# Optimization experiments

Measured on AMD Instinct MI355X. Metric: run time of the kernel, lower is better.

Reference implementation:

```python
import jax, jax.numpy as jnp
import numpy as np

C = 512
NUM_GROUPS = 32
EPS = 1e-6


def setup_inputs() -> dict:
    key = jax.random.key(0)
    ks = jax.random.split(key, 10)
    x = jax.random.normal(ks[0], (2, C, 64, 64), dtype=jnp.float32)
    s = 1.0 / np.sqrt(C)
    return {
        "x": x,
        "gn_gamma": jnp.ones((C,), jnp.float32),
        "gn_beta": jnp.zeros((C,), jnp.float32),
        "wq": jax.random.normal(ks[1], (C, C), jnp.float32) * s,
        "bq": jnp.zeros((C,), jnp.float32),
        "wk": jax.random.normal(ks[2], (C, C), jnp.float32) * s,
        "bk": jnp.zeros((C,), jnp.float32),
        "wv": jax.random.normal(ks[3], (C, C), jnp.float32) * s,
        "bv": jnp.zeros((C,), jnp.float32),
        "wo": jax.random.normal(ks[4], (C, C), jnp.float32) * s,
        "bo": jnp.zeros((C,), jnp.float32),
    }


def group_norm(x, gamma, beta):
    b, c, h, w = x.shape
    xg = x.reshape(b, NUM_GROUPS, c // NUM_GROUPS, h, w)
    mean = xg.mean(axis=(2, 3, 4), keepdims=True)
    var = xg.var(axis=(2, 3, 4), keepdims=True)
    xg = (xg - mean) * jax.lax.rsqrt(var + EPS)
    x = xg.reshape(b, c, h, w)
    return x * gamma[None, :, None, None] + beta[None, :, None, None]


def conv1x1(x, w, bias):
    # 1x1 conv == channel matmul: (b,c,h,w),(o,c) -> (b,o,h,w)
    return jnp.einsum('bchw,oc->bohw', x, w) + bias[None, :, None, None]


def reference(x, gn_gamma, gn_beta, wq, bq, wk, bk, wv, bv, wo, bo):
    b, c, h, w = x.shape
    hn = group_norm(x, gn_gamma, gn_beta)
    q = conv1x1(hn, wq, bq).reshape(b, c, h * w)  # (b,c,n)
    k = conv1x1(hn, wk, bk).reshape(b, c, h * w)
    v = conv1x1(hn, wv, bv).reshape(b, c, h * w)
    scale = int(c) ** (-0.5)
    # scores[b,i,j] = sum_c q[b,c,i] k[b,c,j]
    scores = jnp.einsum('bci,bcj->bij', q, k) * scale
    attn = jax.nn.softmax(scores, axis=2)
    out = jnp.einsum('bcj,bij->bci', v, attn).reshape(b, c, h, w)
    out = conv1x1(out, wo, bo)
    return x + out
```

## Files before the change

### kernel.cpp

```cpp
#include <hip/hip_runtime.h>

typedef unsigned short ushort_t;
typedef unsigned char uchar_t;
typedef __bf16 bf16x8 __attribute__((ext_vector_type(8)));
typedef float f32x4 __attribute__((ext_vector_type(4)));

__device__ __forceinline__ ushort_t f2bf(float f) {
  unsigned u = __float_as_uint(f);
  u += 0x7fff + ((u >> 16) & 1);
  return (ushort_t)(u >> 16);
}

__device__ __forceinline__ void gload16(const void* g, void* l) {
  __builtin_amdgcn_global_load_lds(
      (const __attribute__((address_space(1))) unsigned int*)g,
      (__attribute__((address_space(3))) unsigned int*)l, 16, 0, 0);
}

__global__ __launch_bounds__(256) void cvt_weights(
    const float* __restrict__ wq, const float* __restrict__ wk,
    const float* __restrict__ wv, const float* __restrict__ wo,
    const float* __restrict__ bq, const float* __restrict__ bk,
    ushort_t* __restrict__ dst, float* __restrict__ qkbias,
    float* __restrict__ stats2) {
  int b = blockIdx.x, t = threadIdx.x;
  if (b < 1024) {
    int i = b * 256 + t;
    dst[i]          = f2bf(wq[i]);
    dst[262144 + i] = f2bf(wk[i]);
    dst[524288 + i] = f2bf(wv[i]);
    dst[786432 + i] = f2bf(wo[i]);
  } else if (b < 1028) {
    int j = (b - 1024) * 256 + t;
    qkbias[j] = (j < 512) ? bq[j] : bk[j - 512];
  } else {
    if (t < 128) stats2[t] = 0.f;
  }
}

__global__ __launch_bounds__(256) void zero_f32(float* __restrict__ p) {
  p[blockIdx.x * 256 + threadIdx.x] = 0.f;
}

__global__ __launch_bounds__(256) void gn_stats_partial(const float* __restrict__ x,
                                                        float* __restrict__ stats2) {
  int bg = blockIdx.x >> 2, q = blockIdx.x & 3;
  const float4* p = (const float4*)(x + (size_t)bg * 65536 + q * 16384);
  float s = 0.f, ss = 0.f;
  for (int i = threadIdx.x; i < 4096; i += 256) {
    float4 v = p[i];
    s += v.x + v.y + v.z + v.w;
    ss += v.x * v.x + v.y * v.y + v.z * v.z + v.w * v.w;
  }
  for (int off = 32; off; off >>= 1) {
    s += __shfl_xor(s, off, 64);
    ss += __shfl_xor(ss, off, 64);
  }
  __shared__ float sh[8];
  int wave = threadIdx.x >> 6, lane = threadIdx.x & 63;
  if (lane == 0) { sh[wave] = s; sh[4 + wave] = ss; }
  __syncthreads();
  if (threadIdx.x == 0) {
    atomicAdd(&stats2[bg * 2], sh[0] + sh[1] + sh[2] + sh[3]);
    atomicAdd(&stats2[bg * 2 + 1], sh[4] + sh[5] + sh[6] + sh[7]);
  }
}

__global__ __launch_bounds__(64) void gn_finalize(const float* __restrict__ stats2,
                                                  float* __restrict__ stats) {
  int t = threadIdx.x;
  float s = stats2[t * 2], ss = stats2[t * 2 + 1];
  float mean = s * (1.f / 65536.f);
  float var = ss * (1.f / 65536.f) - mean * mean;
  stats[t * 2] = mean;
  stats[t * 2 + 1] = rsqrtf(var + 1e-6f);
}

__global__ __launch_bounds__(256) void gn_apply(
    const float* __restrict__ x, const float* __restrict__ gamma,
    const float* __restrict__ beta, const float* __restrict__ stats,
    ushort_t* __restrict__ hnT) {
  __shared__ float T[32][33];
  int i0 = blockIdx.x * 32, c0 = blockIdx.y * 32, b = blockIdx.z;
  int tx = threadIdx.x, ty = threadIdx.y;
#pragma unroll
  for (int k = 0; k < 4; k++) {
    int cl = ty + k * 8;
    int c = c0 + cl;
    int bg = (b * 32 + (c >> 4)) * 2;
    float mean = stats[bg], rstd = stats[bg + 1];
    float v = x[((size_t)(b * 512 + c)) * 4096 + i0 + tx];
    T[cl][tx] = (v - mean) * rstd * gamma[c] + beta[c];
  }
  __syncthreads();
#pragma unroll
  for (int k = 0; k < 4; k++) {
    int il = ty + k * 8;
    hnT[((size_t)b * 4096 + i0 + il) * 512 + c0 + tx] = f2bf(T[tx][il]);
  }
}

template <int BN, int UNR>
__global__ __launch_bounds__(256) void gemm_abt(
    const ushort_t* __restrict__ A, long long sA, int lda,
    const ushort_t* __restrict__ B, long long sB, int ldb,
    int K, int N, int ldc,
    ushort_t* __restrict__ outB, long long sC,
    const float* __restrict__ bias, int bias_mode, float scale,
    float* __restrict__ outF, const float* __restrict__ resid,
    float* __restrict__ rowsum, const float* __restrict__ colscale,
    int swiz, int omode) {
  constexpr int CPW = (8 + BN / 16) / 4;
  constexpr int SB = (128 + BN) * 32;
  constexpr int STEP = 32 * UNR;
  constexpr int MI = (BN == 128) ? 4 : 2;
  constexpr int NI = 4;
  __shared__ __align__(16) ushort_t Ls[2][UNR * SB];

  int bx = blockIdx.x, by = blockIdx.y, bz = blockIdx.z;
  if (swiz) {
    unsigned nx = gridDim.x, ny = gridDim.y;
    unsigned id = (blockIdx.z * ny + blockIdx.y) * nx + blockIdx.x;
    unsigned pb8 = (nx * ny) >> 3;
    unsigned c = id & 7, j = id >> 3;
    bz = j / pb8;
    unsigned jb = j - bz * pb8;
    unsigned jy = jb / nx;
    by = c * (ny >> 3) + jy;
    bx = jb - jy * nx;
  }

  int m0 = by * 128, n0 = bx * BN;
  int t = threadIdx.x;
  int lane = t & 63;
  int quad = lane >> 4, l16 = lane & 15;
  int wave = t >> 6;
  int wm = (BN == 128) ? (wave >> 1) * 64 : wave * 32;
  int wn = (BN == 128) ? (wave & 1) * 64 : 0;

  f32x4 acc[MI][NI];
#pragma unroll
  for (int i = 0; i < MI; i++)
#pragma unroll
    for (int j = 0; j < NI; j++)
#pragma unroll
      for (int r = 0; r < 4; r++) acc[i][j][r] = 0.f;

  const ushort_t* gp[CPW];
  int lofs[CPW];
  int crow = lane >> 2, skoff = (lane & 3) * 8;
#pragma unroll
  for (int i = 0; i < CPW; i++) {
    int c = wave * CPW + i;
    if (c < 8) {
      gp[i] = A + (size_t)bz * sA + (size_t)(m0 + c * 16 + crow) * lda + skoff;
      lofs[i] = c * 1024 + lane * 16;
    } else {
      int slot = (c - 8) * 16 + crow;
      int arow = (slot & ~63) + ((slot & 15) * 4) + ((slot & 63) >> 4);
      gp[i] = B + (size_t)bz * sB + (size_t)(n0 + arow) * ldb + skoff;
      lofs[i] = 8192 + (c - 8) * 1024 + lane * 16;
    }
  }
  char* lbase = (char*)&Ls[0][0];

#pragma unroll
  for (int s = 0; s < UNR; s++)
#pragma unroll
    for (int i = 0; i < CPW; i++)
      gload16(gp[i] + s * 32, lbase + s * (SB * 2) + lofs[i]);

  for (int k0 = 0; k0 < K; k0 += STEP) {
    int p = (k0 / STEP) & 1;
    __syncthreads();
    if (k0 + STEP < K) {
      int pofs = (p ^ 1) * (UNR * SB * 2);
#pragma unroll
      for (int s = 0; s < UNR; s++)
#pragma unroll
        for (int i = 0; i < CPW; i++)
          gload16(gp[i] + k0 + STEP + s * 32, lbase + pofs + s * (SB * 2) + lofs[i]);
    }
#pragma unroll
    for (int s = 0; s < UNR; s++) {
      bf16x8 af[MI], bfr[NI];
#pragma unroll
      for (int i = 0; i < MI; i++)
        af[i] = *(const bf16x8*)&Ls[p][s * SB + (wm + i * 16 + l16) * 32 + quad * 8];
#pragma unroll
      for (int j = 0; j < NI; j++)
        bfr[j] = *(const bf16x8*)&Ls[p][s * SB + 4096 + (wn + j * 16 + l16) * 32 + quad * 8];
#pragma unroll
      for (int mi = 0; mi < MI; mi++)
#pragma unroll
        for (int ni = 0; ni < NI; ni++)
          acc[mi][ni] = __builtin_amdgcn_mfma_f32_16x16x32_bf16(af[mi], bfr[ni], acc[mi][ni], 0, 0, 0);
    }
  }

  size_t cbase = (size_t)bz * sC;
  int gnb = n0 + wn + l16 * 4;
  float cs4[4] = {1.f, 1.f, 1.f, 1.f};
  if (colscale) {
    float4 c4 = *(const float4*)&colscale[(size_t)bz * N + gnb];
    cs4[0] = 1.f / c4.x; cs4[1] = 1.f / c4.y; cs4[2] = 1.f / c4.z; cs4[3] = 1.f / c4.w;
  }
  float b4[4] = {0.f, 0.f, 0.f, 0.f};
  if (bias_mode == 2) {
    float4 t4 = *(const float4*)&bias[gnb];
    b4[0] = t4.x; b4[1] = t4.y; b4[2] = t4.z; b4[3] = t4.w;
  }
#pragma unroll
  for (int mi = 0; mi < MI; mi++) {
#pragma unroll
    for (int r = 0; r < 4; r++) {
      int m = m0 + wm + mi * 16 + quad * 4 + r;
      float rbias = (bias_mode == 1) ? bias[m] : 0.f;
      float v4[4];
      float rs = 0.f;
#pragma unroll
      for (int ni = 0; ni < NI; ni++) {
        float val = acc[mi][ni][r];
        if (colscale) val *= cs4[ni];
        val += (bias_mode == 2) ? b4[ni] : rbias;
        val *= scale;
        if (rowsum) { val = __expf(val) * 0.0625f; rs += val; }
        v4[ni] = val;
      }
      size_t idx = cbase + (size_t)m * ldc + gnb;
      if (omode == 1) {
        float4 rv = *(const float4*)&resid[idx];
        float4 ov = make_float4(v4[0] + rv.x, v4[1] + rv.y, v4[2] + rv.z, v4[3] + rv.w);
        *(float4*)&outF[idx] = ov;
      } else if (omode == 2) {
        unsigned w = __builtin_amdgcn_cvt_pk_fp8_f32(v4[0], v4[1], 0u, false);
        w = __builtin_amdgcn_cvt_pk_fp8_f32(v4[2], v4[3], w, true);
        *(unsigned*)&((uchar_t*)outB)[idx] = w;
      } else {
        unsigned lo = (unsigned)f2bf(v4[0]) | ((unsigned)f2bf(v4[1]) << 16);
        unsigned hi = (unsigned)f2bf(v4[2]) | ((unsigned)f2bf(v4[3]) << 16);
        *(uint2*)&outB[idx] = make_uint2(lo, hi);
      }
      if (rowsum) {
        rs += __shfl_xor(rs, 1, 64);
        rs += __shfl_xor(rs, 2, 64);
        rs += __shfl_xor(rs, 4, 64);
        rs += __shfl_xor(rs, 8, 64);
        if (l16 == 0) atomicAdd(&rowsum[(size_t)bz * 4096 + m], rs);
      }
    }
  }
}

template <int BN>
__global__ __launch_bounds__(256) void gemm_fp8(
    const uchar_t* __restrict__ A, long long sA, int lda,
    const uchar_t* __restrict__ B, long long sB, int ldb,
    int K, int ldc,
    void* __restrict__ outp, long long sC,
    float scale, float* __restrict__ rowsum, int swiz, int omode) {
  constexpr int SBB = (128 + BN) * 128;
  constexpr int BASEB = 128 * 128;
  constexpr int NL = SBB / 4096;
  constexpr int MI = (BN == 128) ? 4 : 2;
  constexpr int NI = 4;
  __shared__ __align__(16) uchar_t Ls[2][SBB];

  int bx = blockIdx.x, by = blockIdx.y, bz = blockIdx.z;
  if (swiz) {
    unsigned nx = gridDim.x, ny = gridDim.y;
    unsigned id = (blockIdx.z * ny + blockIdx.y) * nx + blockIdx.x;
    unsigned pb8 = (nx * ny) >> 3;
    unsigned c = id & 7, j = id >> 3;
    bz = j / pb8;
    unsigned jb = j - bz * pb8;
    unsigned jy = jb / nx;
    by = c * (ny >> 3) + jy;
    bx = jb - jy * nx;
  }

  int m0 = by * 128, n0 = bx * BN;
  int t = threadIdx.x;
  int lane = t & 63;
  int quad = lane >> 4, l16 = lane & 15;
  int wave = t >> 6;
  int wm = (BN == 128) ? (wave >> 1) * 64 : wave * 32;
  int wn = (BN == 128) ? (wave & 1) * 64 : 0;

  f32x4 acc[MI][NI];
#pragma unroll
  for (int i = 0; i < MI; i++)
#pragma unroll
    for (int j = 0; j < NI; j++)
#pragma unroll
      for (int r = 0; r < 4; r++) acc[i][j][r] = 0.f;

  const uchar_t* gp[NL];
  int lofs[NL];
#pragma unroll
  for (int i = 0; i < NL; i++) {
    int o = i * 4096 + t * 16;
    int row = o >> 7;
    int kb = (o & 127) ^ ((row & 7) << 4);
    if (row < 128) {
      gp[i] = A + (size_t)bz * sA + (size_t)(m0 + row) * lda + kb;
    } else {
      int br = row - 128;
      int g = br & ~63, loc = br & 63;
      int ar = g + (loc & 15) * 4 + (loc >> 4);
      gp[i] = B + (size_t)bz * sB + (size_t)(n0 + ar) * ldb + kb;
    }
    lofs[i] = o;
  }
  char* lbase = (char*)&Ls[0][0];

  const int NT = K >> 7;
#pragma unroll
  for (int i = 0; i < NL; i++) gload16(gp[i], lbase + lofs[i]);
#pragma unroll
  for (int i = 0; i < NL; i++) gload16(gp[i] + 128, lbase + SBB + lofs[i]);

  int swz = (l16 & 7) << 4;
  for (int kt = 0; kt < NT; ++kt) {
    if (kt < NT - 1) {
      if constexpr (BN == 128)
        asm volatile("s_waitcnt vmcnt(8)" ::: "memory");
      else
        asm volatile("s_waitcnt vmcnt(6)" ::: "memory");
    } else {
      asm volatile("s_waitcnt vmcnt(0)" ::: "memory");
    }
    __builtin_amdgcn_s_barrier();
    const uchar_t* Lp = &Ls[kt & 1][0];
    __builtin_amdgcn_s_setprio(1);
#pragma unroll
    for (int ks = 0; ks < 4; ks++) {
      int kx = (ks * 32 + quad * 8) ^ swz;
      long long af[MI], bfv[NI];
#pragma unroll
      for (int i = 0; i < MI; i++)
        af[i] = *(const long long*)&Lp[(wm + i * 16 + l16) * 128 + kx];
#pragma unroll
      for (int j = 0; j < NI; j++)
        bfv[j] = *(const long long*)&Lp[BASEB + (wn + j * 16 + l16) * 128 + kx];
#pragma unroll
      for (int mi = 0; mi < MI; mi++)
#pragma unroll
        for (int ni = 0; ni < NI; ni++)
          acc[mi][ni] = __builtin_amdgcn_mfma_f32_16x16x32_fp8_fp8(af[mi], bfv[ni], acc[mi][ni], 0, 0, 0);
    }
    __builtin_amdgcn_s_setprio(0);
    if (kt + 2 < NT) {
      asm volatile("s_waitcnt lgkmcnt(0)" ::: "memory");
      __builtin_amdgcn_sched_barrier(0);
      __builtin_amdgcn_s_barrier();
      int pofs = (kt & 1) * SBB;
      int ko = (kt + 2) * 128;
#pragma unroll
      for (int i = 0; i < NL; i++)
        gload16(gp[i] + ko, lbase + pofs + lofs[i]);
    }
  }

  size_t cbase = (size_t)bz * sC;
  int gnb = n0 + wn + l16 * 4;
#pragma unroll
  for (int mi = 0; mi < MI; mi++) {
#pragma unroll
    for (int r = 0; r < 4; r++) {
      int m = m0 + wm + mi * 16 + quad * 4 + r;
      if (omode == 2) {
        float v4[4];
        float rs = 0.f;
#pragma unroll
        for (int ni = 0; ni < NI; ni++) {
          v4[ni] = __expf(acc[mi][ni][r] * scale) * 0.0625f;
          rs += v4[ni];
        }
        unsigned w = __builtin_amdgcn_cvt_pk_fp8_f32(v4[0], v4[1], 0u, false);
        w = __builtin_amdgcn_cvt_pk_fp8_f32(v4[2], v4[3], w, true);
        *(unsigned*)&((uchar_t*)outp)[cbase + (size_t)m * ldc + gnb] = w;
        rs += __shfl_xor(rs, 1, 64);
        rs += __shfl_xor(rs, 2, 64);
        rs += __shfl_xor(rs, 4, 64);
        rs += __shfl_xor(rs, 8, 64);
        if (l16 == 0) atomicAdd(&rowsum[(size_t)bz * 4096 + m], rs);
      } else {
        unsigned lo = (unsigned)f2bf(acc[mi][0][r]) | ((unsigned)f2bf(acc[mi][1][r]) << 16);
        unsigned hi = (unsigned)f2bf(acc[mi][2][r]) | ((unsigned)f2bf(acc[mi][3][r]) << 16);
        *(uint2*)&((ushort_t*)outp)[cbase + (size_t)m * ldc + gnb] = make_uint2(lo, hi);
      }
    }
  }
}

extern "C" void kernel_launch(void* const* d_in, const int* in_sizes, int n_in,
                              void* d_out, int out_size, void* d_ws, size_t ws_size,
                              hipStream_t stream) {
  const float* x     = (const float*)d_in[0];
  const float* gamma = (const float*)d_in[1];
  const float* beta  = (const float*)d_in[2];
  const float* wq    = (const float*)d_in[3];
  const float* bq    = (const float*)d_in[4];
  const float* wk    = (const float*)d_in[5];
  const float* bk    = (const float*)d_in[6];
  const float* wv    = (const float*)d_in[7];
  const float* bv    = (const float*)d_in[8];
  const float* wo    = (const float*)d_in[9];
  const float* bo    = (const float*)d_in[10];
  float* out = (float*)d_out;

  ushort_t* wb  = (ushort_t*)d_ws;
  ushort_t* wvb = wb + 524288;
  ushort_t* wob = wb + 786432;
  ushort_t* hnT = wb + 1048576;
  uchar_t*  qk8 = (uchar_t*)(hnT + 4194304);
  uchar_t*  vC8 = qk8 + 8388608;
  ushort_t* OT  = (ushort_t*)(vC8 + 4194304);
  uchar_t*  S8  = (uchar_t*)(OT + 4194304);
  float* fbuf   = (float*)(S8 + 33554432);
  float* stats  = fbuf;
  float* stats2 = fbuf + 128;
  float* qkbias = fbuf + 256;
  float* l      = (float*)hnT;

  const long long HS = 2097152;
  const long long QS = 4194304;
  const long long SS = 16777216;
  const float scale = 0.044194173824159216f;

  cvt_weights<<<dim3(1029), dim3(256), 0, stream>>>(wq, wk, wv, wo, bq, bk, wb, qkbias, stats2);
  gn_stats_partial<<<dim3(256), dim3(256), 0, stream>>>(x, stats2);
  gn_finalize<<<dim3(1), dim3(64), 0, stream>>>(stats2, stats);
  gn_apply<<<dim3(128, 16, 2), dim3(32, 8), 0, stream>>>(x, gamma, beta, stats, hnT);
  gemm_abt<128, 2><<<dim3(8, 32, 2), dim3(256), 0, stream>>>(
      hnT, HS, 512, wb, 0, 512, 512, 1024, 1024, (ushort_t*)qk8, QS, qkbias, 2, 1.f,
      nullptr, nullptr, nullptr, nullptr, 1, 2);
  gemm_abt<64, 2><<<dim3(64, 4, 2), dim3(256), 0, stream>>>(
      wvb, 0, 512, hnT, HS, 512, 512, 4096, 4096, (ushort_t*)vC8, HS, bv, 1, 1.f,
      nullptr, nullptr, nullptr, nullptr, 0, 2);
  zero_f32<<<dim3(32), dim3(256), 0, stream>>>(l);
  gemm_fp8<128><<<dim3(32, 32, 2), dim3(256), 0, stream>>>(
      qk8, QS, 1024, qk8 + 512, QS, 1024, 512, 4096, S8, SS, scale, l, 1, 2);
  gemm_fp8<64><<<dim3(8, 32, 2), dim3(256), 0, stream>>>(
      S8, SS, 4096, vC8, HS, 4096, 4096, 512, OT, HS, 1.f, nullptr, 1, 0);
  gemm_abt<64, 2><<<dim3(64, 4, 2), dim3(256), 0, stream>>>(
      wob, 0, 512, OT, HS, 512, 512, 4096, 4096, nullptr, HS, bo, 1, 1.f,
      out, x, nullptr, l, 0, 1);
}
```

Before: 231.5 us.

## Split fp8 attention GEMM into specialized QK and PV kernels with 256-row tiles

Result: slower. 259.0 us (+11.9%).

```diff
diff --git a/kernel.cpp b/kernel.cpp
--- a/kernel.cpp
+++ b/kernel.cpp
@@ -252,48 +252,161 @@
   }
 }
 
-template <int BN>
-__global__ __launch_bounds__(256) void gemm_fp8(
+__global__ __launch_bounds__(256) void gemm_qk(
     const uchar_t* __restrict__ A, long long sA, int lda,
     const uchar_t* __restrict__ B, long long sB, int ldb,
-    int K, int ldc,
-    void* __restrict__ outp, long long sC,
-    float scale, float* __restrict__ rowsum, int swiz, int omode) {
-  constexpr int SBB = (128 + BN) * 128;
-  constexpr int BASEB = 128 * 128;
-  constexpr int NL = SBB / 4096;
-  constexpr int MI = (BN == 128) ? 4 : 2;
-  constexpr int NI = 4;
+    int K, int ldc, uchar_t* __restrict__ outp, long long sC,
+    float scale, float* __restrict__ rowsum) {
+  constexpr int ABY = 16384;
+  constexpr int SBB = ABY + 8192;
+  constexpr int CPW = 6;
   __shared__ __align__(16) uchar_t Ls[2][SBB];
 
-  int bx = blockIdx.x, by = blockIdx.y, bz = blockIdx.z;
-  if (swiz) {
-    unsigned nx = gridDim.x, ny = gridDim.y;
-    unsigned id = (blockIdx.z * ny + blockIdx.y) * nx + blockIdx.x;
-    unsigned pb8 = (nx * ny) >> 3;
-    unsigned c = id & 7, j = id >> 3;
-    bz = j / pb8;
-    unsigned jb = j - bz * pb8;
-    unsigned jy = jb / nx;
-    by = c * (ny >> 3) + jy;
-    bx = jb - jy * nx;
-  }
-
-  int m0 = by * 128, n0 = bx * BN;
+  unsigned nx = gridDim.x, ny = gridDim.y;
+  unsigned id = (blockIdx.z * ny + blockIdx.y) * nx + blockIdx.x;
+  unsigned pb8 = (nx * ny) >> 3;
+  unsigned cc = id & 7, j = id >> 3;
+  int bz = j / pb8;
+  unsigned jb = j - bz * pb8;
+  unsigned jy = jb / nx;
+  int by = cc * (ny >> 3) + jy;
+  int bx = jb - jy * nx;
+
+  int m0 = by * 256, n0 = bx * 128;
   int t = threadIdx.x;
   int lane = t & 63;
   int quad = lane >> 4, l16 = lane & 15;
   int wave = t >> 6;
-  int wm = (BN == 128) ? (wave >> 1) * 64 : wave * 32;
-  int wn = (BN == 128) ? (wave & 1) * 64 : 0;
-
-  f32x4 acc[MI][NI];
-#pragma unroll
-  for (int i = 0; i < MI; i++)
-#pragma unroll
-    for (int j = 0; j < NI; j++)
-#pragma unroll
-      for (int r = 0; r < 4; r++) acc[i][j][r] = 0.f;
+  int wm = (wave >> 1) * 64, wn = (wave & 1) * 64;
+
+  f32x4 acc[2][4][4];
+#pragma unroll
+  for (int h = 0; h < 2; h++)
+#pragma unroll
+    for (int i = 0; i < 4; i++)
+#pragma unroll
+      for (int j4 = 0; j4 < 4; j4++)
+#pragma unroll
+        for (int r = 0; r < 4; r++) acc[h][i][j4][r] = 0.f;
+
+  const uchar_t* gp[CPW];
+  int lofs[CPW];
+  int r16 = lane & 15, sseg = quad * 16;
+#pragma unroll
+  for (int i = 0; i < CPW; i++) {
+    int c = wave * CPW + i;
+    if (c < 16) {
+      gp[i] = A + (size_t)bz * sA + (size_t)(m0 + c * 16 + r16) * lda + sseg;
+      lofs[i] = c * 1024 + lane * 16;
+    } else {
+      int cb = c - 16;
+      int slot = cb * 16 + r16;
+      int arow = (slot & ~63) + ((slot & 15) * 4) + ((slot & 63) >> 4);
+      gp[i] = B + (size_t)bz * sB + (size_t)(n0 + arow) * ldb + sseg;
+      lofs[i] = ABY + cb * 1024 + lane * 16;
+    }
+  }
+  char* lbase = (char*)&Ls[0][0];
+
+#pragma unroll
+  for (int i = 0; i < CPW; i++) gload16(gp[i], lbase + lofs[i]);
+
+  int vbase = l16 * 16 + (quad >> 1) * 256 + (quad & 1) * 8;
+  for (int k0 = 0; k0 < K; k0 += 64) {
+    int p = (k0 >> 6) & 1;
+    __syncthreads();
+    if (k0 + 64 < K) {
+      int pofs = (p ^ 1) * SBB;
+#pragma unroll
+      for (int i = 0; i < CPW; i++)
+        gload16(gp[i] + k0 + 64, lbase + pofs + lofs[i]);
+    }
+    const uchar_t* Lp = &Ls[p][0];
+#pragma unroll
+    for (int s = 0; s < 2; s++) {
+      long long af[2][4], bfv[4];
+#pragma unroll
+      for (int h = 0; h < 2; h++)
+#pragma unroll
+        for (int i = 0; i < 4; i++)
+          af[h][i] = *(const long long*)&Lp[h * 8192 + wm * 64 + i * 1024 + s * 512 + vbase];
+#pragma unroll
+      for (int j4 = 0; j4 < 4; j4++)
+        bfv[j4] = *(const long long*)&Lp[ABY + wn * 64 + j4 * 1024 + s * 512 + vbase];
+#pragma unroll
+      for (int h = 0; h < 2; h++)
+#pragma unroll
+        for (int mi = 0; mi < 4; mi++)
+#pragma unroll
+          for (int ni = 0; ni < 4; ni++)
+            acc[h][mi][ni] = __builtin_amdgcn_mfma_f32_16x16x32_fp8_fp8(af[h][mi], bfv[ni], acc[h][mi][ni], 0, 0, 0);
+    }
+  }
+
+  size_t cbase = (size_t)bz * sC;
+  int gnb = n0 + wn + l16 * 4;
+#pragma unroll
+  for (int h = 0; h < 2; h++) {
+#pragma unroll
+    for (int mi = 0; mi < 4; mi++) {
+#pragma unroll
+      for (int r = 0; r < 4; r++) {
+        int m = m0 + h * 128 + wm + mi * 16 + quad * 4 + r;
+        float v4[4];
+        float rs = 0.f;
+#pragma unroll
+        for (int ni = 0; ni < 4; ni++) {
+          v4[ni] = __expf(acc[h][mi][ni][r] * scale) * 0.0625f;
+          rs += v4[ni];
+        }
+        unsigned w = __builtin_amdgcn_cvt_pk_fp8_f32(v4[0], v4[1], 0u, false);
+        w = __builtin_amdgcn_cvt_pk_fp8_f32(v4[2], v4[3], w, true);
+        *(unsigned*)&outp[cbase + (size_t)m * ldc + gnb] = w;
+        rs += __shfl_xor(rs, 1, 64);
+        rs += __shfl_xor(rs, 2, 64);
+        rs += __shfl_xor(rs, 4, 64);
+        rs += __shfl_xor(rs, 8, 64);
+        if (l16 == 0) atomicAdd(&rowsum[(size_t)bz * 4096 + m], rs);
+      }
+    }
+  }
+}
+
+__global__ __launch_bounds__(256) void gemm_pv(
+    const uchar_t* __restrict__ A, long long sA, int lda,
+    const uchar_t* __restrict__ B, long long sB, int ldb,
+    int K, int ldc, ushort_t* __restrict__ outp, long long sC) {
+  constexpr int BASEB = 32768;
+  constexpr int SBB = BASEB + 8192;
+  constexpr int NL = SBB / 4096;
+  __shared__ __align__(16) uchar_t Ls[2][SBB];
+
+  unsigned nx = gridDim.x, ny = gridDim.y;
+  unsigned id = (blockIdx.z * ny + blockIdx.y) * nx + blockIdx.x;
+  unsigned pb8 = (nx * ny) >> 3;
+  unsigned cc = id & 7, j = id >> 3;
+  int bz = j / pb8;
+  unsigned jb = j - bz * pb8;
+  unsigned jy = jb / nx;
+  int by = cc * (ny >> 3) + jy;
+  int bx = jb - jy * nx;
+
+  int m0 = by * 256, n0 = bx * 64;
+  int t = threadIdx.x;
+  int lane = t & 63;
+  int quad = lane >> 4, l16 = lane & 15;
+  int wave = t >> 6;
+  int wm = wave * 32;
+
+  f32x4 acc[2][2][4];
+#pragma unroll
+  for (int h = 0; h < 2; h++)
+#pragma unroll
+    for (int i = 0; i < 2; i++)
+#pragma unroll
+      for (int j4 = 0; j4 < 4; j4++)
+#pragma unroll
+        for (int r = 0; r < 4; r++) acc[h][i][j4][r] = 0.f;
 
   const uchar_t* gp[NL];
   int lofs[NL];
@@ -302,12 +415,11 @@
     int o = i * 4096 + t * 16;
     int row = o >> 7;
     int kb = (o & 127) ^ ((row & 7) << 4);
-    if (row < 128) {
+    if (row < 256) {
       gp[i] = A + (size_t)bz * sA + (size_t)(m0 + row) * lda + kb;
     } else {
-      int br = row - 128;
-      int g = br & ~63, loc = br & 63;
-      int ar = g + (loc & 15) * 4 + (loc >> 4);
+      int br = row - 256;
+      int ar = (br & 15) * 4 + (br >> 4);
       gp[i] = B + (size_t)bz * sB + (size_t)(n0 + ar) * ldb + kb;
     }
     lofs[i] = o;
@@ -322,32 +434,32 @@
 
   int swz = (l16 & 7) << 4;
   for (int kt = 0; kt < NT; ++kt) {
-    if (kt < NT - 1) {
-      if constexpr (BN == 128)
-        asm volatile("s_waitcnt vmcnt(8)" ::: "memory");
-      else
-        asm volatile("s_waitcnt vmcnt(6)" ::: "memory");
-    } else {
+    if (kt < NT - 1)
+      asm volatile("s_waitcnt vmcnt(10)" ::: "memory");
+    else
       asm volatile("s_waitcnt vmcnt(0)" ::: "memory");
-    }
     __builtin_amdgcn_s_barrier();
     const uchar_t* Lp = &Ls[kt & 1][0];
     __builtin_amdgcn_s_setprio(1);
 #pragma unroll
     for (int ks = 0; ks < 4; ks++) {
       int kx = (ks * 32 + quad * 8) ^ swz;
-      long long af[MI], bfv[NI];
-#pragma unroll
-      for (int i = 0; i < MI; i++)
-        af[i] = *(const long long*)&Lp[(wm + i * 16 + l16) * 128 + kx];
-#pragma unroll
-      for (int j = 0; j < NI; j++)
-        bfv[j] = *(const long long*)&Lp[BASEB + (wn + j * 16 + l16) * 128 + kx];
-#pragma unroll
-      for (int mi = 0; mi < MI; mi++)
-#pragma unroll
-        for (int ni = 0; ni < NI; ni++)
-          acc[mi][ni] = __builtin_amdgcn_mfma_f32_16x16x32_fp8_fp8(af[mi], bfv[ni], acc[mi][ni], 0, 0, 0);
+      long long af[2][2], bfv[4];
+#pragma unroll
+      for (int h = 0; h < 2; h++)
+#pragma unroll
+        for (int i = 0; i < 2; i++)
+          af[h][i] = *(const long long*)&Lp[(h * 128 + wm + i * 16 + l16) * 128 + kx];
+#pragma unroll
+      for (int j4 = 0; j4 < 4; j4++)
+        bfv[j4] = *(const long long*)&Lp[BASEB + (j4 * 16 + l16) * 128 + kx];
+#pragma unroll
+      for (int h = 0; h < 2; h++)
+#pragma unroll
+        for (int mi = 0; mi < 2; mi++)
+#pragma unroll
+          for (int ni = 0; ni < 4; ni++)
+            acc[h][mi][ni] = __builtin_amdgcn_mfma_f32_16x16x32_fp8_fp8(af[h][mi], bfv[ni], acc[h][mi][ni], 0, 0, 0);
     }
     __builtin_amdgcn_s_setprio(0);
     if (kt + 2 < NT) {
@@ -363,32 +475,17 @@
   }
 
   size_t cbase = (size_t)bz * sC;
-  int gnb = n0 + wn + l16 * 4;
-#pragma unroll
-  for (int mi = 0; mi < MI; mi++) {
-#pragma unroll
-    for (int r = 0; r < 4; r++) {
-      int m = m0 + wm + mi * 16 + quad * 4 + r;
-      if (omode == 2) {
-        float v4[4];
-        float rs = 0.f;
-#pragma unroll
-        for (int ni = 0; ni < NI; ni++) {
-          v4[ni] = __expf(acc[mi][ni][r] * scale) * 0.0625f;
-          rs += v4[ni];
-        }
-        unsigned w = __builtin_amdgcn_cvt_pk_fp8_f32(v4[0], v4[1], 0u, false);
-        w = __builtin_amdgcn_cvt_pk_fp8_f32(v4[2], v4[3], w, true);
-        *(unsigned*)&((uchar_t*)outp)[cbase + (size_t)m * ldc + gnb] = w;
-        rs += __shfl_xor(rs, 1, 64);
-        rs += __shfl_xor(rs, 2, 64);
-        rs += __shfl_xor(rs, 4, 64);
-        rs += __shfl_xor(rs, 8, 64);
-        if (l16 == 0) atomicAdd(&rowsum[(size_t)bz * 4096 + m], rs);
-      } else {
-        unsigned lo = (unsigned)f2bf(acc[mi][0][r]) | ((unsigned)f2bf(acc[mi][1][r]) << 16);
-        unsigned hi = (unsigned)f2bf(acc[mi][2][r]) | ((unsigned)f2bf(acc[mi][3][r]) << 16);
-        *(uint2*)&((ushort_t*)outp)[cbase + (size_t)m * ldc + gnb] = make_uint2(lo, hi);
+  int gnb = n0 + l16 * 4;
+#pragma unroll
+  for (int h = 0; h < 2; h++) {
+#pragma unroll
+    for (int mi = 0; mi < 2; mi++) {
+#pragma unroll
+      for (int r = 0; r < 4; r++) {
+        int m = m0 + h * 128 + wm + mi * 16 + quad * 4 + r;
+        unsigned lo = (unsigned)f2bf(acc[h][mi][0][r]) | ((unsigned)f2bf(acc[h][mi][1][r]) << 16);
+        unsigned hi = (unsigned)f2bf(acc[h][mi][2][r]) | ((unsigned)f2bf(acc[h][mi][3][r]) << 16);
+        *(uint2*)&outp[cbase + (size_t)m * ldc + gnb] = make_uint2(lo, hi);
       }
     }
   }
@@ -440,10 +537,10 @@
       wvb, 0, 512, hnT, HS, 512, 512, 4096, 4096, (ushort_t*)vC8, HS, bv, 1, 1.f,
       nullptr, nullptr, nullptr, nullptr, 0, 2);
   zero_f32<<<dim3(32), dim3(256), 0, stream>>>(l);
-  gemm_fp8<128><<<dim3(32, 32, 2), dim3(256), 0, stream>>>(
-      qk8, QS, 1024, qk8 + 512, QS, 1024, 512, 4096, S8, SS, scale, l, 1, 2);
-  gemm_fp8<64><<<dim3(8, 32, 2), dim3(256), 0, stream>>>(
-      S8, SS, 4096, vC8, HS, 4096, 4096, 512, OT, HS, 1.f, nullptr, 1, 0);
+  gemm_qk<<<dim3(32, 16, 2), dim3(256), 0, stream>>>(
+      qk8, QS, 1024, qk8 + 512, QS, 1024, 512, 4096, S8, SS, scale, l);
+  gemm_pv<<<dim3(8, 16, 2), dim3(256), 0, stream>>>(
+      S8, SS, 4096, vC8, HS, 4096, 4096, 512, OT, HS);
   gemm_abt<64, 2><<<dim3(64, 4, 2), dim3(256), 0, stream>>>(
       wob, 0, 512, OT, HS, 512, 512, 4096, 4096, nullptr, HS, bo, 1, 1.f,
       out, x, nullptr, l, 0, 1);
```

## Add dedicated 256x64 fp8 PV GEMM kernel with larger M tile

Applied to the files above, without the earlier changes.

Result: slower. 237.6 us (+2.6%).

```diff
diff --git a/kernel.cpp b/kernel.cpp
--- a/kernel.cpp
+++ b/kernel.cpp
@@ -394,6 +394,125 @@
   }
 }
 
+__global__ __launch_bounds__(256) void gemm_pv(
+    const uchar_t* __restrict__ A, long long sA, int lda,
+    const uchar_t* __restrict__ B, long long sB, int ldb,
+    int K, int ldc, ushort_t* __restrict__ outp, long long sC) {
+  constexpr int BASEB = 32768;
+  constexpr int SBB = BASEB + 8192;
+  constexpr int NL = SBB / 4096;
+  __shared__ __align__(16) uchar_t Ls[2][SBB];
+
+  unsigned nx = gridDim.x, ny = gridDim.y;
+  unsigned id = (blockIdx.z * ny + blockIdx.y) * nx + blockIdx.x;
+  unsigned pb8 = (nx * ny) >> 3;
+  unsigned cc = id & 7, j = id >> 3;
+  int bz = j / pb8;
+  unsigned jb = j - bz * pb8;
+  unsigned jy = jb / nx;
+  int by = cc * (ny >> 3) + jy;
+  int bx = jb - jy * nx;
+
+  int m0 = by * 256, n0 = bx * 64;
+  int t = threadIdx.x;
+  int lane = t & 63;
+  int quad = lane >> 4, l16 = lane & 15;
+  int wave = t >> 6;
+  int wm = wave * 32;
+
+  f32x4 acc[2][2][4];
+#pragma unroll
+  for (int h = 0; h < 2; h++)
+#pragma unroll
+    for (int i = 0; i < 2; i++)
+#pragma unroll
+      for (int j4 = 0; j4 < 4; j4++)
+#pragma unroll
+        for (int r = 0; r < 4; r++) acc[h][i][j4][r] = 0.f;
+
+  const uchar_t* gp[NL];
+  int lofs[NL];
+#pragma unroll
+  for (int i = 0; i < NL; i++) {
+    int o = i * 4096 + t * 16;
+    int row = o >> 7;
+    int kb = (o & 127) ^ ((row & 7) << 4);
+    if (row < 256) {
+      gp[i] = A + (size_t)bz * sA + (size_t)(m0 + row) * lda + kb;
+    } else {
+      int br = row - 256;
+      int ar = (br & 15) * 4 + (br >> 4);
+      gp[i] = B + (size_t)bz * sB + (size_t)(n0 + ar) * ldb + kb;
+    }
+    lofs[i] = o;
+  }
+  char* lbase = (char*)&Ls[0][0];
+
+  const int NT = K >> 7;
+#pragma unroll
+  for (int i = 0; i < NL; i++) gload16(gp[i], lbase + lofs[i]);
+#pragma unroll
+  for (int i = 0; i < NL; i++) gload16(gp[i] + 128, lbase + SBB + lofs[i]);
+
+  int swz = (l16 & 7) << 4;
+  for (int kt = 0; kt < NT; ++kt) {
+    if (kt < NT - 1)
+      asm volatile("s_waitcnt vmcnt(10)" ::: "memory");
+    else
+      asm volatile("s_waitcnt vmcnt(0)" ::: "memory");
+    __builtin_amdgcn_s_barrier();
+    const uchar_t* Lp = &Ls[kt & 1][0];
+    __builtin_amdgcn_s_setprio(1);
+#pragma unroll
+    for (int ks = 0; ks < 4; ks++) {
+      int kx = (ks * 32 + quad * 8) ^ swz;
+      long long af[2][2], bfv[4];
+#pragma unroll
+      for (int h = 0; h < 2; h++)
+#pragma unroll
+        for (int i = 0; i < 2; i++)
+          af[h][i] = *(const long long*)&Lp[(h * 128 + wm + i * 16 + l16) * 128 + kx];
+#pragma unroll
+      for (int j4 = 0; j4 < 4; j4++)
+        bfv[j4] = *(const long long*)&Lp[BASEB + (j4 * 16 + l16) * 128 + kx];
+#pragma unroll
+      for (int h = 0; h < 2; h++)
+#pragma unroll
+        for (int mi = 0; mi < 2; mi++)
+#pragma unroll
+          for (int ni = 0; ni < 4; ni++)
+            acc[h][mi][ni] = __builtin_amdgcn_mfma_f32_16x16x32_fp8_fp8(af[h][mi], bfv[ni], acc[h][mi][ni], 0, 0, 0);
+    }
+    __builtin_amdgcn_s_setprio(0);
+    if (kt + 2 < NT) {
+      asm volatile("s_waitcnt lgkmcnt(0)" ::: "memory");
+      __builtin_amdgcn_sched_barrier(0);
+      __builtin_amdgcn_s_barrier();
+      int pofs = (kt & 1) * SBB;
+      int ko = (kt + 2) * 128;
+#pragma unroll
+      for (int i = 0; i < NL; i++)
+        gload16(gp[i] + ko, lbase + pofs + lofs[i]);
+    }
+  }
+
+  size_t cbase = (size_t)bz * sC;
+  int gnb = n0 + l16 * 4;
+#pragma unroll
+  for (int h = 0; h < 2; h++) {
+#pragma unroll
+    for (int mi = 0; mi < 2; mi++) {
+#pragma unroll
+      for (int r = 0; r < 4; r++) {
+        int m = m0 + h * 128 + wm + mi * 16 + quad * 4 + r;
+        unsigned lo = (unsigned)f2bf(acc[h][mi][0][r]) | ((unsigned)f2bf(acc[h][mi][1][r]) << 16);
+        unsigned hi = (unsigned)f2bf(acc[h][mi][2][r]) | ((unsigned)f2bf(acc[h][mi][3][r]) << 16);
+        *(uint2*)&outp[cbase + (size_t)m * ldc + gnb] = make_uint2(lo, hi);
+      }
+    }
+  }
+}
+
 extern "C" void kernel_launch(void* const* d_in, const int* in_sizes, int n_in,
                               void* d_out, int out_size, void* d_ws, size_t ws_size,
                               hipStream_t stream) {
@@ -442,8 +561,8 @@
   zero_f32<<<dim3(32), dim3(256), 0, stream>>>(l);
   gemm_fp8<128><<<dim3(32, 32, 2), dim3(256), 0, stream>>>(
       qk8, QS, 1024, qk8 + 512, QS, 1024, 512, 4096, S8, SS, scale, l, 1, 2);
-  gemm_fp8<64><<<dim3(8, 32, 2), dim3(256), 0, stream>>>(
-      S8, SS, 4096, vC8, HS, 4096, 4096, 512, OT, HS, 1.f, nullptr, 1, 0);
+  gemm_pv<<<dim3(8, 16, 2), dim3(256), 0, stream>>>(
+      S8, SS, 4096, vC8, HS, 4096, 4096, 512, OT, HS);
   gemm_abt<64, 2><<<dim3(64, 4, 2), dim3(256), 0, stream>>>(
       wob, 0, 512, OT, HS, 512, 512, 4096, 4096, nullptr, HS, bo, 1, 1.f,
       out, x, nullptr, l, 0, 1);
```
